# Optimization experiments

Measured on AMD Instinct MI355X. Metric: run time of the kernel, lower is better.

The kernel has to match this reference:

```python
import jax, jax.numpy as jnp
import numpy as np

N_HEADS = 32
N_KV = 8
N_REP = N_HEADS // N_KV  # 4
HEAD_DIM = 128
DIM = 4096


def _rope(x, cos, sin, start_pos):
    # x: (B, H, T, hd); cos/sin: (max_seq, hd//2)
    T = x.shape[2]
    c = jax.lax.dynamic_slice_in_dim(cos, start_pos, T, axis=0)[None, None]  # (1,1,T,hd/2)
    s = jax.lax.dynamic_slice_in_dim(sin, start_pos, T, axis=0)[None, None]
    x1, x2 = x[..., : HEAD_DIM // 2], x[..., HEAD_DIM // 2:]
    return jnp.concatenate([x1 * c - x2 * s, x2 * c + x1 * s], axis=-1)


def setup_inputs() -> dict:
    key = jax.random.key(0)
    ks = jax.random.split(key, 7)
    B, T = 1, 2048
    sc = 0.02
    return {
        "x": jax.random.normal(ks[0], (B, T, DIM), jnp.float32),
        "cos": jax.random.normal(ks[1], (T, HEAD_DIM // 2), jnp.float32),
        "sin": jax.random.normal(ks[2], (T, HEAD_DIM // 2), jnp.float32),
        "wq": jax.random.normal(ks[3], (N_HEADS * HEAD_DIM, DIM), jnp.float32) * sc,
        "wk": jax.random.normal(ks[4], (N_KV * HEAD_DIM, DIM), jnp.float32) * sc,
        "wv": jax.random.normal(ks[5], (N_KV * HEAD_DIM, DIM), jnp.float32) * sc,
        "wo": jax.random.normal(ks[6], (DIM, DIM), jnp.float32) * sc,
        "start_pos": 0,
    }


def reference(x, cos, sin, wq, wk, wv, wo, start_pos):
    B, T, _ = x.shape
    # Projections (nn.Linear: y = x @ W^T)
    q = (x @ wq.T).reshape(B, T, N_HEADS, HEAD_DIM).transpose(0, 2, 1, 3)  # (B,Hq,T,hd)
    k = (x @ wk.T).reshape(B, T, N_KV, HEAD_DIM).transpose(0, 2, 1, 3)    # (B,Hk,T,hd)
    v = (x @ wv.T).reshape(B, T, N_KV, HEAD_DIM).transpose(0, 2, 1, 3)
    q = _rope(q, cos, sin, start_pos)
    k = _rope(k, cos, sin, start_pos)
    # GQA: group query heads per kv head instead of materializing repeat_kv
    qg = q.reshape(B, N_KV, N_REP, T, HEAD_DIM)
    scale = 1.0 / jnp.sqrt(jnp.float32(HEAD_DIM))
    scores = jnp.einsum('bgrqd,bgkd->bgrqk', qg, k) * scale  # (B,Hk,rep,T,T)
    causal = jnp.tril(jnp.ones((T, T), dtype=bool))
    scores = jnp.where(causal, scores, jnp.finfo(scores.dtype).min)
    attn = jax.nn.softmax(scores, axis=-1)
    yg = jnp.einsum('bgrqk,bgkd->bgrqd', attn, v)  # (B,Hk,rep,T,hd)
    y = yg.reshape(B, N_HEADS, T, HEAD_DIM).transpose(0, 2, 1, 3).reshape(B, T, DIM)
    return y @ wo.T
```

## Files before the change

### kernel.cpp

```cpp
#include <hip/hip_runtime.h>
#include <hip/hip_bf16.h>
#include <stdint.h>

using bf16 = __hip_bfloat16;
using bf16x8 = __attribute__((ext_vector_type(8))) short;
using f32x4  = __attribute__((ext_vector_type(4))) float;

#define AS1 __attribute__((address_space(1)))
#define AS3 __attribute__((address_space(3)))

__device__ __forceinline__ void async_ld16(const void* g, void* l) {
    __builtin_amdgcn_global_load_lds((const AS1 void*)g, (AS3 void*)l, 16, 0, 0);
}

__device__ __forceinline__ f32x4 mfma_bf16(bf16x8 a, bf16x8 b, f32x4 c) {
    return __builtin_amdgcn_mfma_f32_16x16x32_bf16(a, b, c, 0, 0, 0);
}

__device__ __forceinline__ float sexp(float x) {
    return __expf(fmaxf(x, -80.0f));
}

template<int N> __device__ __forceinline__ float dpp_max16(float x) {
    int xi = __builtin_bit_cast(int, x);
    int yi = __builtin_amdgcn_update_dpp(xi, xi, 0x110 | N, 0xf, 0xf, false);
    return fmaxf(x, __builtin_bit_cast(float, yi));
}
template<int N> __device__ __forceinline__ float dpp_add16(float x) {
    int xi = __builtin_bit_cast(int, x);
    int yi = __builtin_amdgcn_update_dpp(0, xi, 0x110 | N, 0xf, 0xf, true);
    return x + __builtin_bit_cast(float, yi);
}
__device__ __forceinline__ float bcast15(float x) {
    return __builtin_bit_cast(float,
        __builtin_amdgcn_ds_swizzle(__builtin_bit_cast(int, x), 0x01F0));
}
__device__ __forceinline__ float redmax16(float x) {
    x = dpp_max16<1>(x); x = dpp_max16<2>(x);
    x = dpp_max16<4>(x); x = dpp_max16<8>(x);
    return bcast15(x);
}
__device__ __forceinline__ float redsum16(float x) {
    x = dpp_add16<1>(x); x = dpp_add16<2>(x);
    x = dpp_add16<4>(x); x = dpp_add16<8>(x);
    return bcast15(x);
}

template<int N> __device__ __forceinline__ void vmw() {
    if constexpr (N == 0) asm volatile("s_waitcnt vmcnt(0)" ::: "memory");
    else if constexpr (N == 5) asm volatile("s_waitcnt vmcnt(5)" ::: "memory");
    else if constexpr (N == 6) asm volatile("s_waitcnt vmcnt(6)" ::: "memory");
}
template<int N> __device__ __forceinline__ void lgw() {
    if constexpr (N == 0) asm volatile("s_waitcnt lgkmcnt(0)" ::: "memory");
    else if constexpr (N == 7) asm volatile("s_waitcnt lgkmcnt(7)" ::: "memory");
    else if constexpr (N == 8) asm volatile("s_waitcnt lgkmcnt(8)" ::: "memory");
}
#define SCB __builtin_amdgcn_sched_barrier(0)

__device__ __forceinline__ void cvt8(const float* p, bf16* d) {
    float4 lo = *(const float4*)p;
    float4 hi = *(const float4*)(p + 4);
    bf16 t8[8] = {__float2bfloat16(lo.x), __float2bfloat16(lo.y),
                  __float2bfloat16(lo.z), __float2bfloat16(lo.w),
                  __float2bfloat16(hi.x), __float2bfloat16(hi.y),
                  __float2bfloat16(hi.z), __float2bfloat16(hi.w)};
    *(bf16x8*)d = *(const bf16x8*)t8;
}

__global__ __launch_bounds__(256) void cvt4_k(const float* __restrict__ x,  bf16* __restrict__ xb,
                                              const float* __restrict__ wq, bf16* __restrict__ wqb,
                                              const float* __restrict__ wk, bf16* __restrict__ wkb,
                                              const float* __restrict__ wv, bf16* __restrict__ wvb) {
    int stride = gridDim.x * blockDim.x;
    for (int u = blockIdx.x * blockDim.x + threadIdx.x; u < 4194304; u += stride) {
        const float* s; bf16* d; size_t off;
        if (u < 1048576)      { s = x;  d = xb;  off = (size_t)u * 8; }
        else if (u < 3145728) { s = wq; d = wqb; off = (size_t)(u - 1048576) * 8; }
        else if (u < 3670016) { s = wk; d = wkb; off = (size_t)(u - 3145728) * 8; }
        else                  { s = wv; d = wvb; off = (size_t)(u - 3670016) * 8; }
        cvt8(s + off, d + off);
    }
}

__global__ __launch_bounds__(256) void cvt_f32_bf16(const float* __restrict__ src,
                                                    bf16* __restrict__ dst, int n8) {
    int stride = gridDim.x * blockDim.x;
    for (int u = blockIdx.x * blockDim.x + threadIdx.x; u < n8; u += stride)
        cvt8(src + (size_t)u * 8, dst + (size_t)u * 8);
}

template<bool SRCF32>
__device__ __forceinline__ void stage_tile(const void* __restrict__ src,
                                           bf16* __restrict__ s,
                                           int row0, int K, int k0, int tid) {
    if constexpr (SRCF32) {
        const float* g = (const float*)src;
        #pragma unroll
        for (int i = 0; i < 2; ++i) {
            int u = tid + 256 * i;
            int row = u >> 2, c8 = (u & 3) * 8;
            cvt8(g + (size_t)(row0 + row) * K + k0 + c8, &s[row * 32 + c8]);
        }
    } else {
        const bf16* g = (const bf16*)src;
        const int wave = tid >> 6, lane = tid & 63;
        const int c0 = wave * 64 + lane;
        const int r0 = c0 >> 2, cb0 = (c0 & 3) * 16;
        const int c1 = 256 + c0;
        const int r1 = c1 >> 2, cb1 = (c1 & 3) * 16;
        async_ld16((const char*)(g + (size_t)(row0 + r0) * K + k0) + cb0,
                   (char*)s + wave * 1024);
        async_ld16((const char*)(g + (size_t)(row0 + r1) * K + k0) + cb1,
                   (char*)s + 4096 + wave * 1024);
    }
}

template<bool AF32, bool BF32, int MODE>
__global__ __launch_bounds__(256) void gemm_bt(const void* __restrict__ A,
                                               const void* __restrict__ B,
                                               void* __restrict__ C,
                                               bf16* __restrict__ Qp,
                                               bf16* __restrict__ Kp,
                                               bf16* __restrict__ Vp,
                                               int M, int N, int K) {
    __shared__ bf16 sA[128 * 32];
    __shared__ bf16 sB[128 * 32];
    const int tid  = threadIdx.x;
    const int lane = tid & 63;
    const int wave = tid >> 6;
    const int m0 = blockIdx.y * 128;
    const int n0 = blockIdx.x * 128;
    const int mrow = (wave >> 1) * 64;
    const int ncol = (wave & 1) * 64;

    f32x4 acc[4][4] = {};

    for (int k0 = 0; k0 < K; k0 += 32) {
        __syncthreads();
        stage_tile<AF32>(A, sA, m0, K, k0, tid);
        stage_tile<BF32>(B, sB, n0, K, k0, tid);
        __syncthreads();

        bf16x8 af[4], bfr[4];
        #pragma unroll
        for (int i = 0; i < 4; ++i)
            af[i] = *(const bf16x8*)&sA[(mrow + i * 16 + (lane & 15)) * 32 + (lane >> 4) * 8];
        #pragma unroll
        for (int j = 0; j < 4; ++j)
            bfr[j] = *(const bf16x8*)&sB[(ncol + j * 16 + (lane & 15)) * 32 + (lane >> 4) * 8];
        #pragma unroll
        for (int i = 0; i < 4; ++i)
            #pragma unroll
            for (int j = 0; j < 4; ++j)
                acc[i][j] = mfma_bf16(af[i], bfr[j], acc[i][j]);
    }

    #pragma unroll
    for (int i = 0; i < 4; ++i)
        #pragma unroll
        for (int j = 0; j < 4; ++j)
            #pragma unroll
            for (int r = 0; r < 4; ++r) {
                int row = m0 + mrow + i * 16 + (lane >> 4) * 4 + r;
                int col = n0 + ncol + j * 16 + (lane & 15);
                float fv = acc[i][j][r];
                if constexpr (MODE == 0) {
                    ((bf16*)C)[(size_t)row * N + col] = __float2bfloat16(fv);
                } else if constexpr (MODE == 1) {
                    ((bf16*)C)[(size_t)col * M + row] = __float2bfloat16(fv);
                } else if constexpr (MODE == 2) {
                    bf16 v = __float2bfloat16(fv);
                    if (col < 4096)      Qp[(size_t)row * 4096 + col] = v;
                    else if (col < 5120) Kp[(size_t)row * 1024 + (col - 4096)] = v;
                    else                 Vp[(size_t)(col - 5120) * 2048 + row] = v;
                } else {
                    ((float*)C)[(size_t)row * N + col] = fv;
                }
            }
}

#define KTILE(SA, SB, SA2, SB2, T2, DOST, WTN) do {                               \
    bf16x8 aF0[4], bF0[NFr], aF1[4], bF1[NFr];                                    \
    _Pragma("unroll") for (int i = 0; i < 4; ++i)                                 \
        aF0[i] = *(const bf16x8*)((SA) + offA[i][0]);                             \
    _Pragma("unroll") for (int j = 0; j < NFr; ++j)                               \
        bF0[j] = *(const bf16x8*)((SB) + offB[j][0]);                             \
    SCB;                                                                          \
    _Pragma("unroll") for (int i = 0; i < 4; ++i)                                 \
        aF1[i] = *(const bf16x8*)((SA) + offA[i][1]);                             \
    _Pragma("unroll") for (int j = 0; j < NFr; ++j)                               \
        bF1[j] = *(const bf16x8*)((SB) + offB[j][1]);                             \
    SCB;                                                                          \
    if (DOST) { stgA(SA2, T2); stgB(SB2, T2); }                                   \
    lgw<4 + NFr>();                                                               \
    SCB;                                                                          \
    __builtin_amdgcn_s_setprio(1);                                                \
    _Pragma("unroll") for (int i = 0; i < 4; ++i)                                 \
      _Pragma("unroll") for (int j = 0; j < NFr; ++j)                             \
        acc[i][j] = mfma_bf16(aF0[i], bF0[j], acc[i][j]);                         \
    __builtin_amdgcn_s_setprio(0);                                                \
    SCB;                                                                          \
    lgw<0>();                                                                     \
    SCB;                                                                          \
    __builtin_amdgcn_s_setprio(1);                                                \
    _Pragma("unroll") for (int i = 0; i < 4; ++i)                                 \
      _Pragma("unroll") for (int j = 0; j < NFr; ++j)                             \
        acc[i][j] = mfma_bf16(aF1[i], bF1[j], acc[i][j]);                         \
    __builtin_amdgcn_s_setprio(0);                                                \
    SCB;                                                                          \
    vmw<WTN>();                                                                   \
    __builtin_amdgcn_s_barrier();                                                 \
  } while (0)

template<int MODE, int BM, int NWC, int NFr>
__global__ __launch_bounds__(512, 1) void gemm_kt(const bf16* __restrict__ A,
                                                  const bf16* __restrict__ B,
                                                  void* __restrict__ C,
                                                  bf16* __restrict__ Qp,
                                                  bf16* __restrict__ Kp,
                                                  bf16* __restrict__ Vp,
                                                  int M, int N, int K) {
    constexpr int BN  = NWC * NFr * 16;
    constexpr int IA  = BM / 64;
    constexpr int IB  = BN / 64;
    constexpr int IPT = IA + IB;

    __shared__ __align__(16) bf16 sA0[BM * 64], sA1[BM * 64], sA2[BM * 64];
    __shared__ __align__(16) bf16 sB0[BN * 64], sB1[BN * 64], sB2[BN * 64];

    const int tid  = threadIdx.x;
    const int lane = tid & 63;
    const int wave = tid >> 6;
    const int wr   = wave / NWC;
    const int wc   = wave % NWC;
    const int m0 = blockIdx.y * BM;
    const int n0 = blockIdx.x * BN;
    const int NT = K >> 6;

    int offA[4][2], offB[NFr][2];
    {
        const int l15 = lane & 15, l4 = lane >> 4;
        #pragma unroll
        for (int i = 0; i < 4; ++i) {
            const int ra = wr * 64 + i * 16 + l15;
            #pragma unroll
            for (int kh = 0; kh < 2; ++kh)
                offA[i][kh] = ra * 64 + (((kh * 4 + l4) ^ (ra & 7)) * 8);
        }
        #pragma unroll
        for (int j = 0; j < NFr; ++j) {
            const int rb = wc * (NFr * 16) + j * 16 + l15;
            #pragma unroll
            for (int kh = 0; kh < 2; ++kh)
                offB[j][kh] = rb * 64 + (((kh * 4 + l4) ^ (rb & 7)) * 8);
        }
    }

    const int rloc = tid >> 3;
    const int qsw  = (tid & 7) ^ (rloc & 7);
    const bf16* gA[IA];
    const bf16* gB[IB];
    #pragma unroll
    for (int k = 0; k < IA; ++k) gA[k] = A + (size_t)(m0 + k * 64 + rloc) * K + qsw * 8;
    #pragma unroll
    for (int k = 0; k < IB; ++k) gB[k] = B + (size_t)(n0 + k * 64 + rloc) * K + qsw * 8;
    const int w512 = wave * 512;

    auto stgA = [&](bf16* dst, int kt) __attribute__((always_inline)) {
        #pragma unroll
        for (int k = 0; k < IA; ++k)
            async_ld16(gA[k] + kt * 64, dst + k * 4096 + w512);
    };
    auto stgB = [&](bf16* dst, int kt) __attribute__((always_inline)) {
        #pragma unroll
        for (int k = 0; k < IB; ++k)
            async_ld16(gB[k] + kt * 64, dst + k * 4096 + w512);
    };

    f32x4 acc[4][NFr] = {};

    stgA(sA0, 0); stgB(sB0, 0);
    stgA(sA1, 1); stgB(sB1, 1);
    vmw<IPT>();
    __builtin_amdgcn_s_barrier();
    asm volatile("" ::: "memory");
    SCB;

    int t = 0;
    for (; t < NT - 6; t += 3) {
        KTILE(sA0, sB0, sA2, sB2, t + 2, true, IPT);
        KTILE(sA1, sB1, sA0, sB0, t + 3, true, IPT);
        KTILE(sA2, sB2, sA1, sB1, t + 4, true, IPT);
    }
    KTILE(sA0, sB0, sA2, sB2, NT - 2, true,  IPT);
    KTILE(sA1, sB1, sA0, sB0, NT - 1, true,  IPT);
    KTILE(sA2, sB2, sA0, sB0, 0,      false, 0);
    KTILE(sA0, sB0, sA1, sB1, 0,      false, -1);
    asm volatile("s_waitcnt vmcnt(0)" ::: "memory");

    #pragma unroll
    for (int i = 0; i < 4; ++i)
        #pragma unroll
        for (int j = 0; j < NFr; ++j)
            #pragma unroll
            for (int r = 0; r < 4; ++r) {
                int row = m0 + wr * 64 + i * 16 + (lane >> 4) * 4 + r;
                int col = n0 + wc * (NFr * 16) + j * 16 + (lane & 15);
                float fv = acc[i][j][r];
                if constexpr (MODE == 2) {
                    bf16 v = __float2bfloat16(fv);
                    if (col < 4096)      Qp[(size_t)row * 4096 + col] = v;
                    else if (col < 5120) Kp[(size_t)row * 1024 + (col - 4096)] = v;
                    else                 Vp[(size_t)(col - 5120) * 2048 + row] = v;
                } else {
                    ((float*)C)[(size_t)row * N + col] = fv;
                }
            }
}

__global__ __launch_bounds__(256) void rope_all(bf16* __restrict__ Q,
                                                bf16* __restrict__ K,
                                                const float* __restrict__ cosp,
                                                const float* __restrict__ sinp,
                                                const int* __restrict__ spp) {
    int idx = blockIdx.x * blockDim.x + threadIdx.x;
    int d = idx & 63;
    int h = (idx >> 6) % 40;
    int t = idx / (64 * 40);
    int sp = *spp;
    float c = cosp[(size_t)(t + sp) * 64 + d];
    float s = sinp[(size_t)(t + sp) * 64 + d];
    bf16* row = (h < 32) ? (Q + (size_t)t * 4096 + h * 128)
                         : (K + (size_t)t * 1024 + (h - 32) * 128);
    float x1 = __bfloat162float(row[d]);
    float x2 = __bfloat162float(row[64 + d]);
    row[d]      = __float2bfloat16(x1 * c - x2 * s);
    row[64 + d] = __float2bfloat16(x2 * c + x1 * s);
}

#define NEG_SENT (-1.0e9f)
__global__ __launch_bounds__(256) void attn_k2(const bf16* __restrict__ Q,
                                               const bf16* __restrict__ K,
                                               const bf16* __restrict__ VT,
                                               bf16* __restrict__ Y) {
    constexpr int SKS = 136;
    constexpr int SVS = 72;
    __shared__ bf16 sK[64 * SKS];
    __shared__ bf16 sVT[128 * SVS];
    __shared__ bf16 sP[128 * SVS];

    const int tid  = threadIdx.x;
    const int lane = tid & 63;
    const int wave = tid >> 6;
    const int qtile = 15 - (blockIdx.x >> 5);
    const int head  = blockIdx.x & 31;
    const int g     = head >> 2;
    const int qrow0 = qtile * 128 + wave * 32;
    bf16* sPw = sP + wave * 32 * SVS;

    bf16x8 qf[2][4];
    #pragma unroll
    for (int mi = 0; mi < 2; ++mi) {
        const bf16* qbase = Q + (size_t)(qrow0 + mi * 16 + (lane & 15)) * 4096 + head * 128;
        #pragma unroll
        for (int kk = 0; kk < 4; ++kk)
            qf[mi][kk] = *(const bf16x8*)(qbase + kk * 32 + (lane >> 4) * 8);
    }

    float m_i[2][4], l_i[2][4];
    #pragma unroll
    for (int mi = 0; mi < 2; ++mi)
        #pragma unroll
        for (int r = 0; r < 4; ++r) { m_i[mi][r] = NEG_SENT; l_i[mi][r] = 0.f; }
    f32x4 o[2][8] = {};
    const float scale = 0.08838834764831845f;

    const int ktn = 2 * qtile + 2;
    for (int kt = 0; kt < ktn; ++kt) {
        const int kt0 = kt * 64;
        __syncthreads();
        #pragma unroll
        for (int i = 0; i < 4; ++i) {
            int c = i * 256 + tid;
            {
                int row = c >> 4, ch = c & 15;
                *(uint4*)&sK[row * SKS + ch * 8] =
                    *(const uint4*)(K + (size_t)(kt0 + row) * 1024 + g * 128 + ch * 8);
            }
            {
                int row = c >> 3, ch = c & 7;
                *(uint4*)&sVT[row * SVS + ch * 8] =
                    *(const uint4*)(VT + (size_t)(g * 128 + row) * 2048 + kt0 + ch * 8);
            }
        }
        __syncthreads();

        f32x4 s[2][4];
        #pragma unroll
        for (int mi = 0; mi < 2; ++mi)
            #pragma unroll
            for (int j = 0; j < 4; ++j) {
                f32x4 a = {};
                #pragma unroll
                for (int kk = 0; kk < 4; ++kk) {
                    bf16x8 kfrag = *(const bf16x8*)&sK[(j * 16 + (lane & 15)) * SKS +
                                                       kk * 32 + (lane >> 4) * 8];
                    a = mfma_bf16(qf[mi][kk], kfrag, a);
                }
                s[mi][j] = a;
            }

        #pragma unroll
        for (int mi = 0; mi < 2; ++mi)
            #pragma unroll
            for (int j = 0; j < 4; ++j) {
                int tk = kt0 + j * 16 + (lane & 15);
                #pragma unroll
                for (int r = 0; r < 4; ++r) {
                    int tq = qrow0 + mi * 16 + (lane >> 4) * 4 + r;
                    float v = s[mi][j][r] * scale;
                    s[mi][j][r] = (tk > tq) ? NEG_SENT : v;
                }
            }

        #pragma unroll
        for (int mi = 0; mi < 2; ++mi)
            #pragma unroll
            for (int r = 0; r < 4; ++r) {
                float mx = fmaxf(fmaxf(s[mi][0][r], s[mi][1][r]),
                                 fmaxf(s[mi][2][r], s[mi][3][r]));
                mx = redmax16(mx);
                float mn = fmaxf(m_i[mi][r], mx);
                float alpha = sexp(m_i[mi][r] - mn);
                m_i[mi][r] = mn;
                float rs = 0.f;
                #pragma unroll
                for (int j = 0; j < 4; ++j) {
                    float pv = sexp(s[mi][j][r] - mn);
                    s[mi][j][r] = pv;
                    rs += pv;
                }
                l_i[mi][r] = l_i[mi][r] * alpha + rs;
                #pragma unroll
                for (int j2 = 0; j2 < 8; ++j2) o[mi][j2][r] *= alpha;
            }

        #pragma unroll
        for (int mi = 0; mi < 2; ++mi)
            #pragma unroll
            for (int j = 0; j < 4; ++j)
                #pragma unroll
                for (int r = 0; r < 4; ++r)
                    sPw[(mi * 16 + (lane >> 4) * 4 + r) * SVS + j * 16 + (lane & 15)] =
                        __float2bfloat16(s[mi][j][r]);
        __asm__ volatile("s_waitcnt lgkmcnt(0)" ::: "memory");

        #pragma unroll
        for (int kk2 = 0; kk2 < 2; ++kk2) {
            bf16x8 pf[2];
            #pragma unroll
            for (int mi = 0; mi < 2; ++mi)
                pf[mi] = *(const bf16x8*)&sPw[(mi * 16 + (lane & 15)) * SVS +
                                              kk2 * 32 + (lane >> 4) * 8];
            #pragma unroll
            for (int j2 = 0; j2 < 8; ++j2) {
                bf16x8 vf = *(const bf16x8*)&sVT[(j2 * 16 + (lane & 15)) * SVS +
                                                 kk2 * 32 + (lane >> 4) * 8];
                #pragma unroll
                for (int mi = 0; mi < 2; ++mi)
                    o[mi][j2] = mfma_bf16(pf[mi], vf, o[mi][j2]);
            }
        }
    }

    #pragma unroll
    for (int mi = 0; mi < 2; ++mi)
        #pragma unroll
        for (int r = 0; r < 4; ++r) l_i[mi][r] = redsum16(l_i[mi][r]);
    #pragma unroll
    for (int mi = 0; mi < 2; ++mi)
        #pragma unroll
        for (int j2 = 0; j2 < 8; ++j2)
            #pragma unroll
            for (int r = 0; r < 4; ++r) {
                int t   = qrow0 + mi * 16 + (lane >> 4) * 4 + r;
                int col = head * 128 + j2 * 16 + (lane & 15);
                Y[(size_t)t * 4096 + col] = __float2bfloat16(o[mi][j2][r] / l_i[mi][r]);
            }
}

extern "C" void kernel_launch(void* const* d_in, const int* in_sizes, int n_in,
                              void* d_out, int out_size, void* d_ws, size_t ws_size,
                              hipStream_t stream) {
    const float* x    = (const float*)d_in[0];
    const float* cosp = (const float*)d_in[1];
    const float* sinp = (const float*)d_in[2];
    const float* wq   = (const float*)d_in[3];
    const float* wk   = (const float*)d_in[4];
    const float* wv   = (const float*)d_in[5];
    const float* wo   = (const float*)d_in[6];
    const int*   sp   = (const int*)d_in[7];
    float* out = (float*)d_out;

    char* ws = (char*)d_ws;
    bf16* Qb = (bf16*)d_out;

    const size_t NEED = 92274688;
    if (ws_size >= NEED) {
        bf16* xb   = (bf16*)(ws);
        bf16* wqkv = (bf16*)(ws + (16u << 20));
        bf16* wob  = wqkv;
        bf16* Kb   = (bf16*)(ws + (64u << 20));
        bf16* VT   = (bf16*)(ws + (68u << 20));
        bf16* Yb   = (bf16*)(ws + (72u << 20));

        cvt4_k<<<dim3(4096), 256, 0, stream>>>(x, xb, wq, wqkv,
                                               wk, wqkv + 16777216, wv, wqkv + 20971520);

        gemm_kt<2, 128, 4, 3><<<dim3(32, 16), 512, 0, stream>>>(
            xb, wqkv, nullptr, Qb, Kb, VT, 2048, 6144, 4096);

        cvt_f32_bf16<<<dim3(4096), 256, 0, stream>>>(wo, wob, 2097152);

        rope_all<<<dim3(2048 * 40 * 64 / 256), 256, 0, stream>>>(Qb, Kb, cosp, sinp, sp);

        attn_k2<<<dim3(512), 256, 0, stream>>>(Qb, Kb, VT, Yb);

        gemm_kt<3, 256, 2, 4><<<dim3(32, 8), 512, 0, stream>>>(
            Yb, wob, out, nullptr, nullptr, nullptr, 2048, 4096, 4096);
    } else {
        bf16* Kb = (bf16*)(ws);
        bf16* VT = (bf16*)(ws + (4u << 20));
        bf16* Yb = (bf16*)(ws + (8u << 20));

        gemm_bt<true, true, 0><<<dim3(32, 16), 256, 0, stream>>>(
            x, wq, Qb, nullptr, nullptr, nullptr, 2048, 4096, 4096);
        gemm_bt<true, true, 0><<<dim3(8, 16), 256, 0, stream>>>(
            x, wk, Kb, nullptr, nullptr, nullptr, 2048, 1024, 4096);
        gemm_bt<true, true, 1><<<dim3(8, 16), 256, 0, stream>>>(
            x, wv, VT, nullptr, nullptr, nullptr, 2048, 1024, 4096);

        rope_all<<<dim3(2048 * 40 * 64 / 256), 256, 0, stream>>>(Qb, Kb, cosp, sinp, sp);

        attn_k2<<<dim3(512), 256, 0, stream>>>(Qb, Kb, VT, Yb);

        gemm_bt<false, true, 3><<<dim3(32, 16), 256, 0, stream>>>(
            Yb, wo, out, nullptr, nullptr, nullptr, 2048, 4096, 4096);
    }
}
```

Before: 499.7 us.

## Halve attention query tile to 64 rows and alias P buffer onto K LDS

The attention kernel now processes 64 query rows per block, with 16 per wave, instead of 128, and launches 1024 blocks in place of 512. This gives finer causal load balance and lowers register pressure for higher occupancy. The P staging buffer is dropped and aliased onto the K shared tile, which needs an extra barrier per iteration, and s_setprio wraps the MFMA phases. In exchange, each K/V tile is loaded for half as many query rows, which doubles global-to-LDS traffic per query.

```diff
diff --git a/kernel.cpp b/kernel.cpp
--- a/kernel.cpp
+++ b/kernel.cpp
@@ -340,44 +340,39 @@
 }
 
 #define NEG_SENT (-1.0e9f)
-__global__ __launch_bounds__(256) void attn_k2(const bf16* __restrict__ Q,
-                                               const bf16* __restrict__ K,
-                                               const bf16* __restrict__ VT,
-                                               bf16* __restrict__ Y) {
+__global__ __launch_bounds__(256) void attn_k(const bf16* __restrict__ Q,
+                                              const bf16* __restrict__ K,
+                                              const bf16* __restrict__ VT,
+                                              bf16* __restrict__ Y) {
     constexpr int SKS = 136;
     constexpr int SVS = 72;
     __shared__ bf16 sK[64 * SKS];
     __shared__ bf16 sVT[128 * SVS];
-    __shared__ bf16 sP[128 * SVS];
 
     const int tid  = threadIdx.x;
     const int lane = tid & 63;
     const int wave = tid >> 6;
-    const int qtile = 15 - (blockIdx.x >> 5);
+    const int qtile = 31 - (blockIdx.x >> 5);
     const int head  = blockIdx.x & 31;
     const int g     = head >> 2;
-    const int qrow0 = qtile * 128 + wave * 32;
-    bf16* sPw = sP + wave * 32 * SVS;
-
-    bf16x8 qf[2][4];
-    #pragma unroll
-    for (int mi = 0; mi < 2; ++mi) {
-        const bf16* qbase = Q + (size_t)(qrow0 + mi * 16 + (lane & 15)) * 4096 + head * 128;
+    const int qrow0 = qtile * 64 + wave * 16;
+    bf16* sPw = sK + wave * 1152;
+
+    bf16x8 qf[4];
+    {
+        const bf16* qbase = Q + (size_t)(qrow0 + (lane & 15)) * 4096 + head * 128;
         #pragma unroll
         for (int kk = 0; kk < 4; ++kk)
-            qf[mi][kk] = *(const bf16x8*)(qbase + kk * 32 + (lane >> 4) * 8);
-    }
-
-    float m_i[2][4], l_i[2][4];
-    #pragma unroll
-    for (int mi = 0; mi < 2; ++mi)
-        #pragma unroll
-        for (int r = 0; r < 4; ++r) { m_i[mi][r] = NEG_SENT; l_i[mi][r] = 0.f; }
-    f32x4 o[2][8] = {};
+            qf[kk] = *(const bf16x8*)(qbase + kk * 32 + (lane >> 4) * 8);
+    }
+
+    float m_i[4], l_i[4];
+    #pragma unroll
+    for (int r = 0; r < 4; ++r) { m_i[r] = NEG_SENT; l_i[r] = 0.f; }
+    f32x4 o[8] = {};
     const float scale = 0.08838834764831845f;
 
-    const int ktn = 2 * qtile + 2;
-    for (int kt = 0; kt < ktn; ++kt) {
+    for (int kt = 0; kt <= qtile; ++kt) {
         const int kt0 = kt * 64;
         __syncthreads();
         #pragma unroll
@@ -396,98 +391,85 @@
         }
         __syncthreads();
 
-        f32x4 s[2][4];
-        #pragma unroll
-        for (int mi = 0; mi < 2; ++mi)
+        f32x4 s[4];
+        __builtin_amdgcn_s_setprio(1);
+        #pragma unroll
+        for (int j = 0; j < 4; ++j) {
+            f32x4 a = {};
+            #pragma unroll
+            for (int kk = 0; kk < 4; ++kk) {
+                bf16x8 kfrag = *(const bf16x8*)&sK[(j * 16 + (lane & 15)) * SKS +
+                                                   kk * 32 + (lane >> 4) * 8];
+                a = mfma_bf16(qf[kk], kfrag, a);
+            }
+            s[j] = a;
+        }
+        __builtin_amdgcn_s_setprio(0);
+
+        #pragma unroll
+        for (int j = 0; j < 4; ++j) {
+            int tk = kt0 + j * 16 + (lane & 15);
+            #pragma unroll
+            for (int r = 0; r < 4; ++r) {
+                int tq = qrow0 + (lane >> 4) * 4 + r;
+                float v = s[j][r] * scale;
+                s[j][r] = (tk > tq) ? NEG_SENT : v;
+            }
+        }
+
+        #pragma unroll
+        for (int r = 0; r < 4; ++r) {
+            float mx = fmaxf(fmaxf(s[0][r], s[1][r]), fmaxf(s[2][r], s[3][r]));
+            mx = redmax16(mx);
+            float mn = fmaxf(m_i[r], mx);
+            float alpha = sexp(m_i[r] - mn);
+            m_i[r] = mn;
+            float rs = 0.f;
             #pragma unroll
             for (int j = 0; j < 4; ++j) {
-                f32x4 a = {};
-                #pragma unroll
-                for (int kk = 0; kk < 4; ++kk) {
-                    bf16x8 kfrag = *(const bf16x8*)&sK[(j * 16 + (lane & 15)) * SKS +
-                                                       kk * 32 + (lane >> 4) * 8];
-                    a = mfma_bf16(qf[mi][kk], kfrag, a);
-                }
-                s[mi][j] = a;
-            }
-
-        #pragma unroll
-        for (int mi = 0; mi < 2; ++mi)
-            #pragma unroll
-            for (int j = 0; j < 4; ++j) {
-                int tk = kt0 + j * 16 + (lane & 15);
-                #pragma unroll
-                for (int r = 0; r < 4; ++r) {
-                    int tq = qrow0 + mi * 16 + (lane >> 4) * 4 + r;
-                    float v = s[mi][j][r] * scale;
-                    s[mi][j][r] = (tk > tq) ? NEG_SENT : v;
-                }
-            }
-
-        #pragma unroll
-        for (int mi = 0; mi < 2; ++mi)
-            #pragma unroll
-            for (int r = 0; r < 4; ++r) {
-                float mx = fmaxf(fmaxf(s[mi][0][r], s[mi][1][r]),
-                                 fmaxf(s[mi][2][r], s[mi][3][r]));
-                mx = redmax16(mx);
-                float mn = fmaxf(m_i[mi][r], mx);
-                float alpha = sexp(m_i[mi][r] - mn);
-                m_i[mi][r] = mn;
-                float rs = 0.f;
-                #pragma unroll
-                for (int j = 0; j < 4; ++j) {
-                    float pv = sexp(s[mi][j][r] - mn);
-                    s[mi][j][r] = pv;
-                    rs += pv;
-                }
-                l_i[mi][r] = l_i[mi][r] * alpha + rs;
-                #pragma unroll
-                for (int j2 = 0; j2 < 8; ++j2) o[mi][j2][r] *= alpha;
-            }
-
-        #pragma unroll
-        for (int mi = 0; mi < 2; ++mi)
-            #pragma unroll
-            for (int j = 0; j < 4; ++j)
-                #pragma unroll
-                for (int r = 0; r < 4; ++r)
-                    sPw[(mi * 16 + (lane >> 4) * 4 + r) * SVS + j * 16 + (lane & 15)] =
-                        __float2bfloat16(s[mi][j][r]);
+                float pv = sexp(s[j][r] - mn);
+                s[j][r] = pv;
+                rs += pv;
+            }
+            l_i[r] = l_i[r] * alpha + rs;
+            #pragma unroll
+            for (int j2 = 0; j2 < 8; ++j2) o[j2][r] *= alpha;
+        }
+
+        __syncthreads();
+
+        #pragma unroll
+        for (int j = 0; j < 4; ++j)
+            #pragma unroll
+            for (int r = 0; r < 4; ++r)
+                sPw[((lane >> 4) * 4 + r) * SVS + j * 16 + (lane & 15)] =
+                    __float2bfloat16(s[j][r]);
         __asm__ volatile("s_waitcnt lgkmcnt(0)" ::: "memory");
 
+        __builtin_amdgcn_s_setprio(1);
         #pragma unroll
         for (int kk2 = 0; kk2 < 2; ++kk2) {
-            bf16x8 pf[2];
-            #pragma unroll
-            for (int mi = 0; mi < 2; ++mi)
-                pf[mi] = *(const bf16x8*)&sPw[(mi * 16 + (lane & 15)) * SVS +
-                                              kk2 * 32 + (lane >> 4) * 8];
+            bf16x8 pf = *(const bf16x8*)&sPw[(lane & 15) * SVS + kk2 * 32 + (lane >> 4) * 8];
             #pragma unroll
             for (int j2 = 0; j2 < 8; ++j2) {
                 bf16x8 vf = *(const bf16x8*)&sVT[(j2 * 16 + (lane & 15)) * SVS +
                                                  kk2 * 32 + (lane >> 4) * 8];
-                #pragma unroll
-                for (int mi = 0; mi < 2; ++mi)
-                    o[mi][j2] = mfma_bf16(pf[mi], vf, o[mi][j2]);
-            }
-        }
-    }
-
-    #pragma unroll
-    for (int mi = 0; mi < 2; ++mi)
-        #pragma unroll
-        for (int r = 0; r < 4; ++r) l_i[mi][r] = redsum16(l_i[mi][r]);
-    #pragma unroll
-    for (int mi = 0; mi < 2; ++mi)
-        #pragma unroll
-        for (int j2 = 0; j2 < 8; ++j2)
-            #pragma unroll
-            for (int r = 0; r < 4; ++r) {
-                int t   = qrow0 + mi * 16 + (lane >> 4) * 4 + r;
-                int col = head * 128 + j2 * 16 + (lane & 15);
-                Y[(size_t)t * 4096 + col] = __float2bfloat16(o[mi][j2][r] / l_i[mi][r]);
-            }
+                o[j2] = mfma_bf16(pf, vf, o[j2]);
+            }
+        }
+        __builtin_amdgcn_s_setprio(0);
+    }
+
+    #pragma unroll
+    for (int r = 0; r < 4; ++r) l_i[r] = redsum16(l_i[r]);
+    #pragma unroll
+    for (int j2 = 0; j2 < 8; ++j2)
+        #pragma unroll
+        for (int r = 0; r < 4; ++r) {
+            int t   = qrow0 + (lane >> 4) * 4 + r;
+            int col = head * 128 + j2 * 16 + (lane & 15);
+            Y[(size_t)t * 4096 + col] = __float2bfloat16(o[j2][r] / l_i[r]);
+        }
 }
 
 extern "C" void kernel_launch(void* const* d_in, const int* in_sizes, int n_in,
@@ -525,7 +507,7 @@
 
         rope_all<<<dim3(2048 * 40 * 64 / 256), 256, 0, stream>>>(Qb, Kb, cosp, sinp, sp);
 
-        attn_k2<<<dim3(512), 256, 0, stream>>>(Qb, Kb, VT, Yb);
+        attn_k<<<dim3(1024), 256, 0, stream>>>(Qb, Kb, VT, Yb);
 
         gemm_kt<3, 256, 2, 4><<<dim3(32, 8), 512, 0, stream>>>(
             Yb, wob, out, nullptr, nullptr, nullptr, 2048, 4096, 4096);
@@ -543,7 +525,7 @@
 
         rope_all<<<dim3(2048 * 40 * 64 / 256), 256, 0, stream>>>(Qb, Kb, cosp, sinp, sp);
 
-        attn_k2<<<dim3(512), 256, 0, stream>>>(Qb, Kb, VT, Yb);
+        attn_k<<<dim3(1024), 256, 0, stream>>>(Qb, Kb, VT, Yb);
 
         gemm_bt<false, true, 3><<<dim3(32, 16), 256, 0, stream>>>(
             Yb, wo, out, nullptr, nullptr, nullptr, 2048, 4096, 4096);
```

Result: faster. 485.4 us (-2.9%).
